# Kernel optimization log

Measured on AMD Instinct MI355X. Metric: run time of the kernel, lower is better.

Reference implementation:

```python
import jax, jax.numpy as jnp
import numpy as np

B, T, D, H, NHASH, BS, L, DFF = 4, 4096, 512, 8, 4, 64, 4, 2048
DH = D // H           # 64
NB = T // BS          # 64 buckets per hash round
MASK_VAL = -5e4       # TOKEN_SELF_ATTN_VALUE from reformer-pytorch


def setup_inputs() -> dict:
    key = jax.random.key(0)
    ks = jax.random.split(key, 8)
    s = D ** -0.5
    return {
        "src": jax.random.normal(ks[0], (B, T, D), jnp.float32),
        "rotations": jax.random.normal(ks[1], (L, DH, NHASH, NB // 2), jnp.float32),
        "Wqk": jax.random.normal(ks[2], (L, D, D), jnp.float32) * s,
        "Wv": jax.random.normal(ks[3], (L, D, D), jnp.float32) * s,
        "Wout": jax.random.normal(ks[4], (L, D, D), jnp.float32) * s,
        "bout": jnp.zeros((L, D), jnp.float32),
        "W1": jax.random.normal(ks[5], (L, DFF, D), jnp.float32) * s,
        "b1": jnp.zeros((L, DFF), jnp.float32),
        "W2": jax.random.normal(ks[6], (L, D, DFF), jnp.float32) * (DFF ** -0.5),
        "b2": jnp.zeros((L, D), jnp.float32),
        "g2": jnp.ones((L, D), jnp.float32),
        "be2": jnp.zeros((L, D), jnp.float32),
        "gf": jnp.ones((D,), jnp.float32),
        "bf": jnp.zeros((D,), jnp.float32),
    }


def _ln(x, g, b, eps=1e-6):
    m = x.mean(-1, keepdims=True)
    v = ((x - m) ** 2).mean(-1, keepdims=True)
    return (x - m) * jax.lax.rsqrt(v + eps) * g + b


def _look_one_back(x):
    # concat each chunk with the previous chunk along the within-chunk axis
    return jnp.concatenate([x, jnp.roll(x, 1, axis=1)], axis=2)


def _lsh_attention(qk, v, rot):
    # qk, v: (bh, T, DH); rot: (DH, NHASH, NB//2). Shared-QK LSH attention.
    bh = qk.shape[0]
    rotated = jnp.einsum('btf,fhr->bhtr', qk, rot)               # (bh,NHASH,T,NB/2)
    full = jnp.concatenate([rotated, -rotated], axis=-1)          # (bh,NHASH,T,NB)
    buckets = jnp.argmax(full, axis=-1)                           # (bh,NHASH,T)
    buckets = buckets + (jnp.arange(NHASH) * NB)[None, :, None]   # offset per round
    buckets = buckets.reshape(bh, NHASH * T)

    ticker = jnp.arange(NHASH * T)
    bt = buckets * T + (ticker % T)                               # unique sort keys
    sticker = jnp.argsort(bt, axis=-1)                            # sort positions
    undo = jnp.argsort(sticker, axis=-1)
    st = sticker % T                                              # original positions

    sqk = jnp.take_along_axis(qk, st[..., None], axis=1)          # (bh,NHASH*T,DH)
    sv = jnp.take_along_axis(v, st[..., None], axis=1)

    C = NHASH * NB                                                # chunks
    bq_t = st.reshape(bh, C, BS)
    bqk = sqk.reshape(bh, C, BS, DH)
    bv = sv.reshape(bh, C, BS, DH)

    bq = bqk
    bk = bqk / jnp.maximum(jnp.linalg.norm(bqk, axis=-1, keepdims=True), 1e-12)
    bk = _look_one_back(bk)                                       # (bh,C,2*BS,DH)
    bv = _look_one_back(bv)
    bkv_t = _look_one_back(bq_t)                                  # (bh,C,2*BS)

    dots = jnp.einsum('bcie,bcje->bcij', bq, bk) * (DH ** -0.5)   # (bh,C,BS,2BS)
    self_mask = bq_t[:, :, :, None] == bkv_t[:, :, None, :]
    dots = jnp.where(self_mask, MASK_VAL, dots)

    lse = jax.scipy.special.logsumexp(dots, axis=-1, keepdims=True)
    probs = jnp.exp(dots - lse)
    bo = jnp.einsum('bcij,bcje->bcie', probs, bv)                 # (bh,C,BS,DH)

    so = bo.reshape(bh, NHASH * T, DH)
    slog = lse.reshape(bh, NHASH * T)
    o = jnp.take_along_axis(so, undo[..., None], axis=1).reshape(bh, NHASH, T, DH)
    lg = jnp.take_along_axis(slog, undo, axis=1).reshape(bh, NHASH, T, 1)
    w = jnp.exp(lg - jax.scipy.special.logsumexp(lg, axis=1, keepdims=True))
    return jnp.sum(o * w, axis=1)                                 # (bh,T,DH)


def _split_heads(x):
    return x.reshape(B, T, H, DH).transpose(0, 2, 1, 3).reshape(B * H, T, DH)


def _merge_heads(x):
    return x.reshape(B, H, T, DH).transpose(0, 2, 1, 3).reshape(B, T, D)


def reference(src, rotations, Wqk, Wv, Wout, bout, W1, b1, W2, b2, g2, be2, gf, bf):
    x = src
    for i in range(L):
        # LSH self-attention (post-norm path: norm1 is never applied in source)
        qk = _split_heads(x @ Wqk[i].T)
        v = _split_heads(x @ Wv[i].T)
        att = _merge_heads(_lsh_attention(qk, v, rotations[i]))
        att = att @ Wout[i].T + bout[i]
        x = x + att
        # positionalwise FFN + residual + norm2
        ff = jax.nn.relu(x @ W1[i].T + b1[i]) @ W2[i].T + b2[i]
        x = _ln(x + ff, g2[i], be2[i])
    return _ln(x, gf, bf)
```

## Files before the change

kernel.cpp:

```cpp
#include <hip/hip_runtime.h>
#include <math.h>

#define TT    4096
#define DD    512
#define HH    8
#define DHH   64
#define NH    4
#define LLAY  4
#define DFFN  2048
#define BHH   32
#define NC    256
#define MROWS 16384

typedef __attribute__((ext_vector_type(8))) short s16x8;
typedef __attribute__((ext_vector_type(4))) float f32x4;
typedef unsigned short ushort_t;

union U4 { unsigned u[4]; s16x8 v; };

__device__ __forceinline__ unsigned short f2bf(float f) {
    unsigned u = __float_as_uint(f);
    unsigned r = (u + 0x7FFFu + ((u >> 16) & 1u)) >> 16;
    return (unsigned short)r;
}
__device__ __forceinline__ float bf2f(unsigned short h) {
    return __uint_as_float(((unsigned)h) << 16);
}

__device__ __forceinline__ void xcd_swz(int& bx, int& by) {
    const int gx = gridDim.x;
    const int nwg = gx * gridDim.y;
    const int flat = by * gx + bx;
    const int q = nwg >> 3;
    const int swz = (flat & 7) * q + (flat >> 3);
    bx = swz % gx;
    by = swz / gx;
}

__global__ __launch_bounds__(256) void gemm_bf3_k(
    const ushort_t* __restrict__ Ah, const ushort_t* __restrict__ Al, int lda,
    const ushort_t* __restrict__ Wh, const ushort_t* __restrict__ Wl,
    const float* __restrict__ bias, const float* __restrict__ resid,
    float* __restrict__ outf, ushort_t* __restrict__ outh, ushort_t* __restrict__ outl,
    int M, int N, int K, int relu)
{
    __shared__ __align__(16) ushort_t lds[4 * 128 * 32];
    const int tid  = threadIdx.x;
    const int lane = tid & 63;
    const int wv   = tid >> 6;
    const int wm   = wv >> 1, wn = wv & 1;
    int bx = blockIdx.x, by = blockIdx.y;
    xcd_swz(bx, by);
    const int row0 = by * 128, col0 = bx * 128;
    const int g    = lane >> 4;

    f32x4 acc[4][4];
#pragma unroll
    for (int mi = 0; mi < 4; mi++)
#pragma unroll
        for (int ni = 0; ni < 4; ni++) acc[mi][ni] = (f32x4)(0.f);

    const int srow0 = wv * 32;

    for (int k0 = 0; k0 < K; k0 += 32) {
        __syncthreads();
#pragma unroll
        for (int ii = 0; ii < 2; ii++) {
            const int r   = srow0 + ii * 16 + (lane >> 2);
            const int ug  = (((lane & 3) ^ ((r >> 1) & 3)) << 3);
            const size_t ga = (size_t)(row0 + r) * lda + k0 + ug;
            const size_t gw = (size_t)(col0 + r) * K   + k0 + ug;
            const int lo  = (srow0 + ii * 16) * 32;
            __builtin_amdgcn_global_load_lds(
                (const __attribute__((address_space(1))) void*)(Ah + ga),
                (__attribute__((address_space(3))) void*)&lds[0 * 4096 + lo], 16, 0, 0);
            __builtin_amdgcn_global_load_lds(
                (const __attribute__((address_space(1))) void*)(Al + ga),
                (__attribute__((address_space(3))) void*)&lds[1 * 4096 + lo], 16, 0, 0);
            __builtin_amdgcn_global_load_lds(
                (const __attribute__((address_space(1))) void*)(Wh + gw),
                (__attribute__((address_space(3))) void*)&lds[2 * 4096 + lo], 16, 0, 0);
            __builtin_amdgcn_global_load_lds(
                (const __attribute__((address_space(1))) void*)(Wl + gw),
                (__attribute__((address_space(3))) void*)&lds[3 * 4096 + lo], 16, 0, 0);
        }
        __syncthreads();

        s16x8 ah[4], al[4], wh[4], wl[4];
#pragma unroll
        for (int mi = 0; mi < 4; mi++) {
            const int m  = wm * 64 + mi * 16 + (lane & 15);
            const int pu = ((g ^ ((m >> 1) & 3)) << 3);
            ah[mi] = *(const s16x8*)&lds[0 * 4096 + m * 32 + pu];
            al[mi] = *(const s16x8*)&lds[1 * 4096 + m * 32 + pu];
            const int n  = wn * 64 + mi * 16 + (lane & 15);
            const int pn = ((g ^ ((n >> 1) & 3)) << 3);
            wh[mi] = *(const s16x8*)&lds[2 * 4096 + n * 32 + pn];
            wl[mi] = *(const s16x8*)&lds[3 * 4096 + n * 32 + pn];
        }
#pragma unroll
        for (int mi = 0; mi < 4; mi++)
#pragma unroll
            for (int ni = 0; ni < 4; ni++) {
                acc[mi][ni] = __builtin_amdgcn_mfma_f32_16x16x32_bf16(ah[mi], wh[ni], acc[mi][ni], 0, 0, 0);
                acc[mi][ni] = __builtin_amdgcn_mfma_f32_16x16x32_bf16(al[mi], wh[ni], acc[mi][ni], 0, 0, 0);
                acc[mi][ni] = __builtin_amdgcn_mfma_f32_16x16x32_bf16(ah[mi], wl[ni], acc[mi][ni], 0, 0, 0);
            }
    }

#pragma unroll
    for (int mi = 0; mi < 4; mi++) {
#pragma unroll
        for (int ni = 0; ni < 4; ni++) {
#pragma unroll
            for (int r = 0; r < 4; r++) {
                const int row = row0 + wm * 64 + mi * 16 + g * 4 + r;
                const int col = col0 + wn * 64 + ni * 16 + (lane & 15);
                float v = acc[mi][ni][r];
                if (bias)  v += bias[col];
                if (relu)  v = fmaxf(v, 0.f);
                if (resid) v += resid[(size_t)row * N + col];
                if (outf)  outf[(size_t)row * N + col] = v;
                if (outh) {
                    unsigned short h = f2bf(v);
                    outh[(size_t)row * N + col] = h;
                    outl[(size_t)row * N + col] = f2bf(v - bf2f(h));
                }
            }
        }
    }
}

__global__ __launch_bounds__(256) void gemm_bf6_k(
    const ushort_t* __restrict__ A1, const ushort_t* __restrict__ A2,
    const ushort_t* __restrict__ A3, int lda,
    const ushort_t* __restrict__ W1, const ushort_t* __restrict__ W2,
    const ushort_t* __restrict__ W3,
    float* __restrict__ outf, int M, int N, int K)
{
    __shared__ __align__(16) ushort_t lds[6 * 128 * 32];
    const int tid  = threadIdx.x;
    const int lane = tid & 63;
    const int wv   = tid >> 6;
    const int wm   = wv >> 1, wn = wv & 1;
    int bx = blockIdx.x, by = blockIdx.y;
    xcd_swz(bx, by);
    const int row0 = by * 128, col0 = bx * 128;
    const int g    = lane >> 4;

    f32x4 acc[4][4];
#pragma unroll
    for (int mi = 0; mi < 4; mi++)
#pragma unroll
        for (int ni = 0; ni < 4; ni++) acc[mi][ni] = (f32x4)(0.f);

    const int srow0 = wv * 32;

    for (int k0 = 0; k0 < K; k0 += 32) {
        __syncthreads();
#pragma unroll
        for (int ii = 0; ii < 2; ii++) {
            const int r   = srow0 + ii * 16 + (lane >> 2);
            const int ug  = (((lane & 3) ^ ((r >> 1) & 3)) << 3);
            const size_t ga = (size_t)(row0 + r) * lda + k0 + ug;
            const size_t gw = (size_t)(col0 + r) * K   + k0 + ug;
            const int lo  = (srow0 + ii * 16) * 32;
            __builtin_amdgcn_global_load_lds(
                (const __attribute__((address_space(1))) void*)(A1 + ga),
                (__attribute__((address_space(3))) void*)&lds[0 * 4096 + lo], 16, 0, 0);
            __builtin_amdgcn_global_load_lds(
                (const __attribute__((address_space(1))) void*)(A2 + ga),
                (__attribute__((address_space(3))) void*)&lds[1 * 4096 + lo], 16, 0, 0);
            __builtin_amdgcn_global_load_lds(
                (const __attribute__((address_space(1))) void*)(A3 + ga),
                (__attribute__((address_space(3))) void*)&lds[2 * 4096 + lo], 16, 0, 0);
            __builtin_amdgcn_global_load_lds(
                (const __attribute__((address_space(1))) void*)(W1 + gw),
                (__attribute__((address_space(3))) void*)&lds[3 * 4096 + lo], 16, 0, 0);
            __builtin_amdgcn_global_load_lds(
                (const __attribute__((address_space(1))) void*)(W2 + gw),
                (__attribute__((address_space(3))) void*)&lds[4 * 4096 + lo], 16, 0, 0);
            __builtin_amdgcn_global_load_lds(
                (const __attribute__((address_space(1))) void*)(W3 + gw),
                (__attribute__((address_space(3))) void*)&lds[5 * 4096 + lo], 16, 0, 0);
        }
        __syncthreads();

        s16x8 a1[4], a2[4], a3[4], w1[4], w2[4], w3[4];
#pragma unroll
        for (int mi = 0; mi < 4; mi++) {
            const int m  = wm * 64 + mi * 16 + (lane & 15);
            const int pu = ((g ^ ((m >> 1) & 3)) << 3);
            a1[mi] = *(const s16x8*)&lds[0 * 4096 + m * 32 + pu];
            a2[mi] = *(const s16x8*)&lds[1 * 4096 + m * 32 + pu];
            a3[mi] = *(const s16x8*)&lds[2 * 4096 + m * 32 + pu];
            const int n  = wn * 64 + mi * 16 + (lane & 15);
            const int pn = ((g ^ ((n >> 1) & 3)) << 3);
            w1[mi] = *(const s16x8*)&lds[3 * 4096 + n * 32 + pn];
            w2[mi] = *(const s16x8*)&lds[4 * 4096 + n * 32 + pn];
            w3[mi] = *(const s16x8*)&lds[5 * 4096 + n * 32 + pn];
        }
#pragma unroll
        for (int mi = 0; mi < 4; mi++)
#pragma unroll
            for (int ni = 0; ni < 4; ni++) {
                acc[mi][ni] = __builtin_amdgcn_mfma_f32_16x16x32_bf16(a1[mi], w1[ni], acc[mi][ni], 0, 0, 0);
                acc[mi][ni] = __builtin_amdgcn_mfma_f32_16x16x32_bf16(a2[mi], w1[ni], acc[mi][ni], 0, 0, 0);
                acc[mi][ni] = __builtin_amdgcn_mfma_f32_16x16x32_bf16(a1[mi], w2[ni], acc[mi][ni], 0, 0, 0);
                acc[mi][ni] = __builtin_amdgcn_mfma_f32_16x16x32_bf16(a2[mi], w2[ni], acc[mi][ni], 0, 0, 0);
                acc[mi][ni] = __builtin_amdgcn_mfma_f32_16x16x32_bf16(a1[mi], w3[ni], acc[mi][ni], 0, 0, 0);
                acc[mi][ni] = __builtin_amdgcn_mfma_f32_16x16x32_bf16(a3[mi], w1[ni], acc[mi][ni], 0, 0, 0);
            }
    }

#pragma unroll
    for (int mi = 0; mi < 4; mi++) {
#pragma unroll
        for (int ni = 0; ni < 4; ni++) {
#pragma unroll
            for (int r = 0; r < 4; r++) {
                const int row = row0 + wm * 64 + mi * 16 + g * 4 + r;
                const int col = col0 + wn * 64 + ni * 16 + (lane & 15);
                outf[(size_t)row * N + col] = acc[mi][ni][r];
            }
        }
    }
}

__global__ __launch_bounds__(256) void cvt_k(
    const float* __restrict__ in, ushort_t* __restrict__ o1,
    ushort_t* __restrict__ o2, ushort_t* __restrict__ o3, int n4)
{
    int i = blockIdx.x * 256 + threadIdx.x;
    if (i >= n4) return;
    float4 v = ((const float4*)in)[i];
    float vv[4] = {v.x, v.y, v.z, v.w};
    union { unsigned short us[4]; ushort4 v4; } H, L, M;
#pragma unroll
    for (int q = 0; q < 4; q++) {
        unsigned short a = f2bf(vv[q]);
        float r1 = vv[q] - bf2f(a);
        unsigned short b = f2bf(r1);
        H.us[q] = a; L.us[q] = b;
        M.us[q] = f2bf(r1 - bf2f(b));
    }
    ((ushort4*)o1)[i] = H.v4;
    ((ushort4*)o2)[i] = L.v4;
    if (o3) ((ushort4*)o3)[i] = M.v4;
}

__global__ __launch_bounds__(256) void bucket_k(
    const float* __restrict__ qk, const float* __restrict__ rot,
    int* __restrict__ bkt)
{
    __shared__ float rs[NH][64][32];
    const int bh = blockIdx.y;
    const int t = blockIdx.x * 256 + threadIdx.x;
    for (int i = threadIdx.x; i < NH * 64 * 32; i += 256) {
        int r = i >> 11, f = (i >> 5) & 63, j = i & 31;
        rs[r][f][j] = rot[(f * NH + r) * 32 + j];
    }
    __syncthreads();
    const int b = bh >> 3, h = bh & 7;
    const float* q = qk + ((size_t)(b * TT + t)) * DD + h * DHH;
    float qv[64];
#pragma unroll
    for (int f4 = 0; f4 < 16; f4++) {
        float4 tmp = ((const float4*)q)[f4];
        qv[f4 * 4 + 0] = tmp.x; qv[f4 * 4 + 1] = tmp.y;
        qv[f4 * 4 + 2] = tmp.z; qv[f4 * 4 + 3] = tmp.w;
    }
    for (int r = 0; r < NH; r++) {
        float rv[32];
#pragma unroll
        for (int j = 0; j < 32; j++) rv[j] = 0.f;
        for (int f = 0; f < 64; f++) {
            float qf = qv[f];
#pragma unroll
            for (int j = 0; j < 32; j++) rv[j] = fmaf(qf, rs[r][f][j], rv[j]);
        }
        float best = rv[0];
        int bi = 0;
#pragma unroll
        for (int j = 1; j < 32; j++) { if (rv[j] > best) { best = rv[j]; bi = j; } }
#pragma unroll
        for (int j = 0; j < 32; j++) { float v = -rv[j]; if (v > best) { best = v; bi = 32 + j; } }
        bkt[((size_t)bh * NH + r) * TT + t] = bi;
    }
}

__global__ __launch_bounds__(256) void sort_k(
    const int* __restrict__ bkt, int* __restrict__ st)
{
    __shared__ int lb[TT];
    __shared__ unsigned short cnt[128][64];
    __shared__ int base[64];
    const int r = blockIdx.x, bh = blockIdx.y;
    const int tid = threadIdx.x;
    const int* src = bkt + ((size_t)bh * NH + r) * TT;

    const int4* s4 = (const int4*)src;
    int4* l4 = (int4*)lb;
#pragma unroll
    for (int q = 0; q < 4; q++) l4[tid + q * 256] = s4[tid + q * 256];
    unsigned* cz = (unsigned*)cnt;
#pragma unroll
    for (int q = 0; q < 16; q++) cz[tid + q * 256] = 0;
    __syncthreads();

    if (tid < 128) {
        for (int it = 0; it < 32; it++) {
            int bb = lb[tid * 32 + it];
            cnt[tid][bb]++;
        }
    }
    __syncthreads();

    if (tid < 64) {
        const int bb = tid;
        int run = 0;
        for (int s = 0; s < 128; s++) {
            int t = cnt[s][bb];
            cnt[s][bb] = (unsigned short)run;
            run += t;
        }
        int inc = run;
#pragma unroll
        for (int off = 1; off < 64; off <<= 1) {
            int n = __shfl_up(inc, off, 64);
            if (tid >= off) inc += n;
        }
        base[bb] = inc - run;
    }
    __syncthreads();

    if (tid < 128) {
        int* dst = st + (size_t)bh * (NH * TT) + (size_t)r * TT;
        for (int it = 0; it < 32; it++) {
            int t = tid * 32 + it;
            int bb = lb[t];
            int pos = base[bb] + (int)cnt[tid][bb];
            cnt[tid][bb]++;
            dst[pos] = t;
        }
    }
}

__global__ __launch_bounds__(256, 2) void attn_k(
    const float* __restrict__ qk, const float* __restrict__ vbuf,
    const int* __restrict__ st, float* __restrict__ obuf,
    float* __restrict__ lseb, int bh0)
{
    __shared__ __align__(16) ushort_t ksh[128 * 72];
    __shared__ __align__(16) ushort_t ksl[128 * 72];
    __shared__ __align__(16) unsigned vsp[128 * 66];
    __shared__ float invn[128];
    __shared__ int   tks[128];

    const int c   = blockIdx.x;
    const int bhl = blockIdx.y;
    const int bh  = bh0 + bhl;
    const int b   = bh >> 3, h = bh & 7;
    const int tid = threadIdx.x;
    const int* stb = st + (size_t)bh * (NH * TT);

    if (tid < 128) {
        int cc = (tid < 64) ? c : ((c + NC - 1) & (NC - 1));
        tks[tid] = stb[cc * 64 + (tid & 63)];
    }
    __syncthreads();

    {
        const int row = tid >> 1, c0 = (tid & 1) * 32;
        const int t = tks[row];
        const float4* kg = (const float4*)(qk + ((size_t)(b * TT + t)) * DD + h * DHH + c0);
        const float4* vg = (const float4*)(vbuf + ((size_t)(b * TT + t)) * DD + h * DHH + c0);
        float kv[32], vv[32];
        float ss = 0.f;
#pragma unroll
        for (int q = 0; q < 8; q++) {
            float4 kq = kg[q], vq = vg[q];
            kv[4 * q + 0] = kq.x; kv[4 * q + 1] = kq.y; kv[4 * q + 2] = kq.z; kv[4 * q + 3] = kq.w;
            vv[4 * q + 0] = vq.x; vv[4 * q + 1] = vq.y; vv[4 * q + 2] = vq.z; vv[4 * q + 3] = vq.w;
            ss += kq.x * kq.x + kq.y * kq.y + kq.z * kq.z + kq.w * kq.w;
        }
        ss += __shfl_xor(ss, 1);
        if ((tid & 1) == 0) invn[row] = 1.0f / fmaxf(sqrtf(ss), 1e-12f);

        unsigned hw[16], lw[16];
#pragma unroll
        for (int e = 0; e < 16; e++) {
            float a = kv[2 * e], b2 = kv[2 * e + 1];
            unsigned short ha = f2bf(a), hb = f2bf(b2);
            hw[e] = (unsigned)ha | ((unsigned)hb << 16);
            lw[e] = (unsigned)f2bf(a - bf2f(ha)) | ((unsigned)f2bf(b2 - bf2f(hb)) << 16);
        }
        uint4* kdh = (uint4*)&ksh[row * 72 + c0];
        uint4* kdl = (uint4*)&ksl[row * 72 + c0];
#pragma unroll
        for (int q = 0; q < 4; q++) {
            kdh[q] = make_uint4(hw[4 * q], hw[4 * q + 1], hw[4 * q + 2], hw[4 * q + 3]);
            kdl[q] = make_uint4(lw[4 * q], lw[4 * q + 1], lw[4 * q + 2], lw[4 * q + 3]);
        }
        unsigned pw[32];
#pragma unroll
        for (int e = 0; e < 32; e++) {
            unsigned short hv = f2bf(vv[e]);
            pw[e] = (unsigned)hv | ((unsigned)f2bf(vv[e] - bf2f(hv)) << 16);
        }
        uint2* vd = (uint2*)&vsp[row * 66 + c0];
#pragma unroll
        for (int q = 0; q < 16; q++) vd[q] = make_uint2(pw[2 * q], pw[2 * q + 1]);
    }
    __syncthreads();

    const int lane = tid & 63;
    const int wv   = tid >> 6;
    const int cc16 = lane & 15;
    const int g    = lane >> 4;
    const int rr   = c >> 6;

    f32x4 stt[8];
#pragma unroll
    for (int jt = 0; jt < 8; jt++) stt[jt] = (f32x4)(0.f);

    const int qrow = wv * 16 + cc16;
#pragma unroll
    for (int ks = 0; ks < 2; ks++) {
        s16x8 qh = *(const s16x8*)&ksh[qrow * 72 + ks * 32 + g * 8];
        s16x8 ql = *(const s16x8*)&ksl[qrow * 72 + ks * 32 + g * 8];
#pragma unroll
        for (int jt = 0; jt < 8; jt++) {
            const int krow = jt * 16 + cc16;
            s16x8 ah = *(const s16x8*)&ksh[krow * 72 + ks * 32 + g * 8];
            s16x8 al = *(const s16x8*)&ksl[krow * 72 + ks * 32 + g * 8];
            stt[jt] = __builtin_amdgcn_mfma_f32_16x16x32_bf16(ah, qh, stt[jt], 0, 0, 0);
            stt[jt] = __builtin_amdgcn_mfma_f32_16x16x32_bf16(al, qh, stt[jt], 0, 0, 0);
            stt[jt] = __builtin_amdgcn_mfma_f32_16x16x32_bf16(ah, ql, stt[jt], 0, 0, 0);
        }
    }

    const int tqi = tks[wv * 16 + cc16];
    float m = -INFINITY;
#pragma unroll
    for (int jt = 0; jt < 8; jt++) {
#pragma unroll
        for (int r4 = 0; r4 < 4; r4++) {
            const int j = jt * 16 + g * 4 + r4;
            float d = stt[jt][r4] * invn[j] * 0.125f;
            if (tqi == tks[j]) d = -5e4f;
            stt[jt][r4] = d;
            m = fmaxf(m, d);
        }
    }
    m = fmaxf(m, __shfl_xor(m, 16));
    m = fmaxf(m, __shfl_xor(m, 32));
    float s = 0.f;
#pragma unroll
    for (int jt = 0; jt < 8; jt++) {
#pragma unroll
        for (int r4 = 0; r4 < 4; r4++) {
            float e = expf(stt[jt][r4] - m);
            stt[jt][r4] = e;
            s += e;
        }
    }
    s += __shfl_xor(s, 16);
    s += __shfl_xor(s, 32);
    const float is = 1.0f / s;
    if (g == 0) lseb[((size_t)bh * NH + rr) * TT + tqi] = m + logf(s);

    unsigned ph[8][2], pl[8][2];
#pragma unroll
    for (int jt = 0; jt < 8; jt++) {
#pragma unroll
        for (int w2 = 0; w2 < 2; w2++) {
            float p0 = stt[jt][2 * w2] * is;
            float p1 = stt[jt][2 * w2 + 1] * is;
            unsigned short h0 = f2bf(p0), h1 = f2bf(p1);
            ph[jt][w2] = (unsigned)h0 | ((unsigned)h1 << 16);
            pl[jt][w2] = (unsigned)f2bf(p0 - bf2f(h0)) | ((unsigned)f2bf(p1 - bf2f(h1)) << 16);
        }
    }

    f32x4 occ[4];
#pragma unroll
    for (int nt = 0; nt < 4; nt++) occ[nt] = (f32x4)(0.f);

    const int srcLow  = ((g & 1) << 5) + cc16;
    const int srcHigh = srcLow + 16;
    const bool hiT = (lane & 32) != 0;

#pragma unroll
    for (int ks = 0; ks < 4; ks++) {
        U4 Phi, Plo;
        {
            unsigned a0 = (unsigned)__shfl((int)ph[2 * ks][0], srcLow);
            unsigned a1 = (unsigned)__shfl((int)ph[2 * ks][1], srcLow);
            unsigned a2 = (unsigned)__shfl((int)ph[2 * ks][0], srcHigh);
            unsigned a3 = (unsigned)__shfl((int)ph[2 * ks][1], srcHigh);
            unsigned b0 = (unsigned)__shfl((int)ph[2 * ks + 1][0], srcLow);
            unsigned b1 = (unsigned)__shfl((int)ph[2 * ks + 1][1], srcLow);
            unsigned b2 = (unsigned)__shfl((int)ph[2 * ks + 1][0], srcHigh);
            unsigned b3 = (unsigned)__shfl((int)ph[2 * ks + 1][1], srcHigh);
            Phi.u[0] = hiT ? b0 : a0; Phi.u[1] = hiT ? b1 : a1;
            Phi.u[2] = hiT ? b2 : a2; Phi.u[3] = hiT ? b3 : a3;
            unsigned c0 = (unsigned)__shfl((int)pl[2 * ks][0], srcLow);
            unsigned c1 = (unsigned)__shfl((int)pl[2 * ks][1], srcLow);
            unsigned c2 = (unsigned)__shfl((int)pl[2 * ks][0], srcHigh);
            unsigned c3 = (unsigned)__shfl((int)pl[2 * ks][1], srcHigh);
            unsigned d0 = (unsigned)__shfl((int)pl[2 * ks + 1][0], srcLow);
            unsigned d1 = (unsigned)__shfl((int)pl[2 * ks + 1][1], srcLow);
            unsigned d2 = (unsigned)__shfl((int)pl[2 * ks + 1][0], srcHigh);
            unsigned d3 = (unsigned)__shfl((int)pl[2 * ks + 1][1], srcHigh);
            Plo.u[0] = hiT ? d0 : c0; Plo.u[1] = hiT ? d1 : c1;
            Plo.u[2] = hiT ? d2 : c2; Plo.u[3] = hiT ? d3 : c3;
        }
#pragma unroll
        for (int nt = 0; nt < 4; nt++) {
            unsigned u[8];
#pragma unroll
            for (int e = 0; e < 8; e++)
                u[e] = vsp[(32 * ks + 8 * g + e) * 66 + nt * 16 + cc16];
            U4 Vh, Vl;
#pragma unroll
            for (int m2 = 0; m2 < 4; m2++) {
                Vh.u[m2] = (u[2 * m2] & 0xffffu) | (u[2 * m2 + 1] << 16);
                Vl.u[m2] = (u[2 * m2] >> 16) | (u[2 * m2 + 1] & 0xffff0000u);
            }
            occ[nt] = __builtin_amdgcn_mfma_f32_16x16x32_bf16(Phi.v, Vh.v, occ[nt], 0, 0, 0);
            occ[nt] = __builtin_amdgcn_mfma_f32_16x16x32_bf16(Plo.v, Vh.v, occ[nt], 0, 0, 0);
            occ[nt] = __builtin_amdgcn_mfma_f32_16x16x32_bf16(Phi.v, Vl.v, occ[nt], 0, 0, 0);
        }
    }

#pragma unroll
    for (int r4 = 0; r4 < 4; r4++) {
        const int i = wv * 16 + g * 4 + r4;
        const int ti = tks[i];
        float* dst = obuf + (((size_t)bhl * NH + rr) * TT + ti) * DHH + cc16;
        dst[0]  = occ[0][r4];
        dst[16] = occ[1][r4];
        dst[32] = occ[2][r4];
        dst[48] = occ[3][r4];
    }
}

__global__ __launch_bounds__(256) void combine_k(
    const float* __restrict__ obuf, const float* __restrict__ lseb,
    ushort_t* __restrict__ att, int bh0)
{
    int idx = blockIdx.x * 256 + threadIdx.x;
    int d = idx & 63;
    int t = (idx >> 6) & (TT - 1);
    int bhl = idx >> 18;
    int bh = bh0 + bhl;
    float l0 = lseb[((size_t)bh * NH + 0) * TT + t];
    float l1 = lseb[((size_t)bh * NH + 1) * TT + t];
    float l2 = lseb[((size_t)bh * NH + 2) * TT + t];
    float l3 = lseb[((size_t)bh * NH + 3) * TT + t];
    float m = fmaxf(fmaxf(l0, l1), fmaxf(l2, l3));
    float e0 = expf(l0 - m), e1 = expf(l1 - m), e2 = expf(l2 - m), e3 = expf(l3 - m);
    float inv = 1.0f / (e0 + e1 + e2 + e3);
    float o0 = obuf[(((size_t)bhl * NH + 0) * TT + t) * DHH + d];
    float o1 = obuf[(((size_t)bhl * NH + 1) * TT + t) * DHH + d];
    float o2 = obuf[(((size_t)bhl * NH + 2) * TT + t) * DHH + d];
    float o3 = obuf[(((size_t)bhl * NH + 3) * TT + t) * DHH + d];
    float o = (e0 * o0 + e1 * o1 + e2 * o2 + e3 * o3) * inv;
    int b = bh >> 3, h = bh & 7;
    size_t base = (size_t)(b * TT + t) * 1024 + h * DHH + d;
    unsigned short hi = f2bf(o);
    att[base]       = hi;
    att[base + 512] = f2bf(o - bf2f(hi));
}

__global__ __launch_bounds__(64) void ln_k(
    const float* __restrict__ in, const float* __restrict__ g,
    const float* __restrict__ be, float* __restrict__ out,
    ushort_t* __restrict__ oh, ushort_t* __restrict__ ol,
    ushort_t* __restrict__ ol2)
{
    const int row = blockIdx.x;
    const int tid = threadIdx.x;
    const float* x = in + (size_t)row * DD;
    float4 a = *(const float4*)(x + tid * 8);
    float4 b = *(const float4*)(x + tid * 8 + 4);
    float s = a.x + a.y + a.z + a.w + b.x + b.y + b.z + b.w;
#pragma unroll
    for (int o = 32; o >= 1; o >>= 1) s += __shfl_xor(s, o, 64);
    float mean = s * (1.0f / 512.0f);
    float dx[8];
    dx[0] = a.x - mean; dx[1] = a.y - mean; dx[2] = a.z - mean; dx[3] = a.w - mean;
    dx[4] = b.x - mean; dx[5] = b.y - mean; dx[6] = b.z - mean; dx[7] = b.w - mean;
    float ss = 0.f;
#pragma unroll
    for (int q = 0; q < 8; q++) ss += dx[q] * dx[q];
#pragma unroll
    for (int o = 32; o >= 1; o >>= 1) ss += __shfl_xor(ss, o, 64);
    float var = ss * (1.0f / 512.0f);
    float inv = 1.0f / sqrtf(var + 1e-6f);
    const float* gp = g + tid * 8;
    const float* bp = be + tid * 8;
    float y[8];
#pragma unroll
    for (int q = 0; q < 8; q++) y[q] = dx[q] * inv * gp[q] + bp[q];
    float* yp = out + (size_t)row * DD + tid * 8;
    *(float4*)(yp)     = make_float4(y[0], y[1], y[2], y[3]);
    *(float4*)(yp + 4) = make_float4(y[4], y[5], y[6], y[7]);
    if (oh) {
        union { unsigned short us[8]; ushort4 v4[2]; } H, L, M;
#pragma unroll
        for (int q = 0; q < 8; q++) {
            unsigned short h = f2bf(y[q]);
            float r1 = y[q] - bf2f(h);
            unsigned short l = f2bf(r1);
            H.us[q] = h; L.us[q] = l;
            M.us[q] = f2bf(r1 - bf2f(l));
        }
        size_t e = (size_t)row * DD + tid * 8;
        *(ushort4*)(oh + e)      = H.v4[0];
        *(ushort4*)(oh + e + 4)  = H.v4[1];
        *(ushort4*)(ol + e)      = L.v4[0];
        *(ushort4*)(ol + e + 4)  = L.v4[1];
        *(ushort4*)(ol2 + e)     = M.v4[0];
        *(ushort4*)(ol2 + e + 4) = M.v4[1];
    }
}

extern "C" void kernel_launch(void* const* d_in, const int* in_sizes, int n_in,
                              void* d_out, int out_size, void* d_ws, size_t ws_size,
                              hipStream_t stream)
{
    const float* src  = (const float*)d_in[0];
    const float* rots = (const float*)d_in[1];
    const float* Wqk  = (const float*)d_in[2];
    const float* Wv   = (const float*)d_in[3];
    const float* Wout = (const float*)d_in[4];
    const float* bout = (const float*)d_in[5];
    const float* W1   = (const float*)d_in[6];
    const float* b1   = (const float*)d_in[7];
    const float* W2   = (const float*)d_in[8];
    const float* b2   = (const float*)d_in[9];
    const float* g2   = (const float*)d_in[10];
    const float* be2  = (const float*)d_in[11];
    const float* gf   = (const float*)d_in[12];
    const float* bf   = (const float*)d_in[13];
    float* out = (float*)d_out;

    char* w = (char*)d_ws;
    const size_t SZ_X = (size_t)MROWS * DD * 4;
    const size_t XHALF = (size_t)MROWS * DD;
    float*    x     = (float*)(w);
    ushort_t* xs    = (ushort_t*)(w + SZ_X);
    ushort_t* xh    = xs;
    ushort_t* xl    = xs + XHALF;
    ushort_t* xl2   = xs + 2 * XHALF;
    char*     p     = w + SZ_X + 3 * XHALF * 2;
    float*    qkb   = (float*)(p);
    ushort_t* attb  = (ushort_t*)(p);
    float*    vb    = (float*)(p + SZ_X);
    float*    obuf  = (float*)(p + 2 * SZ_X);
    ushort_t* h1b   = (ushort_t*)(p + 2 * SZ_X);
    ushort_t* wb    = (ushort_t*)(p + 4 * SZ_X);
    char*     tail  = p + 4 * SZ_X + 6029312 * 2;
    int*      bkt   = (int*)(tail);
    int*      st    = (int*)(tail + (size_t)BHH * NH * TT * 4);
    float*    lseb  = (float*)(tail + 2 * (size_t)BHH * NH * TT * 4);

    ushort_t* wvh = wb;            ushort_t* wvl = wb + 262144;
    ushort_t* woh = wb + 524288;   ushort_t* wol = wb + 786432;
    ushort_t* w1h = wb + 1048576;  ushort_t* w1l = wb + 2097152;
    ushort_t* w2h = wb + 3145728;  ushort_t* w2l = wb + 4194304;
    ushort_t* wq1 = wb + 5242880;  ushort_t* wq2 = wb + 5505024;
    ushort_t* wq3 = wb + 5767168;
    const size_t H1HALF = (size_t)8192 * DFFN;
    ushort_t* h1h = h1b;           ushort_t* h1l = h1b + H1HALF;

    hipMemcpyAsync(x, src, SZ_X, hipMemcpyDeviceToDevice, stream);
    cvt_k<<<(MROWS * DD / 4 + 255) / 256, 256, 0, stream>>>(src, xh, xl, xl2, MROWS * DD / 4);

    for (int i = 0; i < LLAY; i++) {
        const float* Wqk_i = Wqk + (size_t)i * DD * DD;
        const float* Wv_i  = Wv  + (size_t)i * DD * DD;
        const float* Wout_i= Wout+ (size_t)i * DD * DD;
        const float* bout_i= bout+ (size_t)i * DD;
        const float* W1_i  = W1  + (size_t)i * DFFN * DD;
        const float* b1_i  = b1  + (size_t)i * DFFN;
        const float* W2_i  = W2  + (size_t)i * DD * DFFN;
        const float* b2_i  = b2  + (size_t)i * DD;
        const float* g2_i  = g2  + (size_t)i * DD;
        const float* be2_i = be2 + (size_t)i * DD;
        const float* rot_i = rots + (size_t)i * DHH * NH * 32;

        cvt_k<<<(262144 / 4 + 255) / 256, 256, 0, stream>>>(Wqk_i, wq1, wq2, wq3, 262144 / 4);
        cvt_k<<<(262144 / 4 + 255) / 256, 256, 0, stream>>>(Wv_i, wvh, wvl, nullptr, 262144 / 4);
        cvt_k<<<(262144 / 4 + 255) / 256, 256, 0, stream>>>(Wout_i, woh, wol, nullptr, 262144 / 4);
        cvt_k<<<(1048576 / 4 + 255) / 256, 256, 0, stream>>>(W1_i, w1h, w1l, nullptr, 1048576 / 4);
        cvt_k<<<(1048576 / 4 + 255) / 256, 256, 0, stream>>>(W2_i, w2h, w2l, nullptr, 1048576 / 4);

        gemm_bf6_k<<<dim3(4, 128), 256, 0, stream>>>(xh, xl, xl2, DD, wq1, wq2, wq3,
                                                     qkb, MROWS, DD, DD);
        gemm_bf3_k<<<dim3(4, 128), 256, 0, stream>>>(xh, xl, DD, wvh, wvl,
                                                     nullptr, nullptr, vb, nullptr, nullptr,
                                                     MROWS, DD, DD, 0);
        bucket_k<<<dim3(16, BHH), 256, 0, stream>>>(qkb, rot_i, bkt);
        sort_k<<<dim3(NH, BHH), 256, 0, stream>>>(bkt, st);

        for (int s = 0; s < 2; s++) {
            attn_k<<<dim3(NC, 16), 256, 0, stream>>>(qkb, vb, st, obuf, lseb, s * 16);
            combine_k<<<16384, 256, 0, stream>>>(obuf, lseb, attb, s * 16);
        }

        gemm_bf3_k<<<dim3(4, 128), 256, 0, stream>>>(attb, attb + 512, 1024, woh, wol,
                                                     bout_i, x, x, xh, xl,
                                                     MROWS, DD, DD, 0);
        for (int s = 0; s < 2; s++) {
            const size_t ro = (size_t)s * 8192;
            gemm_bf3_k<<<dim3(16, 64), 256, 0, stream>>>(xh + ro * DD, xl + ro * DD, DD,
                                                         w1h, w1l, b1_i, nullptr,
                                                         nullptr, h1h, h1l,
                                                         8192, DFFN, DD, 1);
            gemm_bf3_k<<<dim3(4, 64), 256, 0, stream>>>(h1h, h1l, DFFN, w2h, w2l,
                                                        b2_i, x + ro * DD,
                                                        vb + ro * DD, nullptr, nullptr,
                                                        8192, DD, DFFN, 0);
        }
        ln_k<<<MROWS, 64, 0, stream>>>(vb, g2_i, be2_i, x, xh, xl, xl2);
    }
    ln_k<<<MROWS, 64, 0, stream>>>(x, gf, bf, out, nullptr, nullptr, nullptr);
}
```

Before: 3.461 ms.

## Split FFN along hidden dimension instead of rows, accumulating second GEMM via residual

The FFN was previously processed in two row halves (8192 rows each, full DFF). It now splits the hidden dimension into two 1024-wide halves over all 16384 rows. The second GEMM of the second half adds onto the first half's output through the residual input. A new leading-dimension parameter for the weight matrix allows strided access into W2 columns. This gives the second GEMM larger grids (4x128 instead of 4x64), which aims to improve occupancy for the K-heavy W2 GEMM. The cost is an extra read-modify-write pass of the fp32 output and a different summation order.

```diff
diff --git a/kernel.cpp b/kernel.cpp
--- a/kernel.cpp
+++ b/kernel.cpp
@@ -39,7 +39,7 @@
 
 __global__ __launch_bounds__(256) void gemm_bf3_k(
     const ushort_t* __restrict__ Ah, const ushort_t* __restrict__ Al, int lda,
-    const ushort_t* __restrict__ Wh, const ushort_t* __restrict__ Wl,
+    const ushort_t* __restrict__ Wh, const ushort_t* __restrict__ Wl, int ldw,
     const float* __restrict__ bias, const float* __restrict__ resid,
     float* __restrict__ outf, ushort_t* __restrict__ outh, ushort_t* __restrict__ outl,
     int M, int N, int K, int relu)
@@ -69,7 +69,7 @@
             const int r   = srow0 + ii * 16 + (lane >> 2);
             const int ug  = (((lane & 3) ^ ((r >> 1) & 3)) << 3);
             const size_t ga = (size_t)(row0 + r) * lda + k0 + ug;
-            const size_t gw = (size_t)(col0 + r) * K   + k0 + ug;
+            const size_t gw = (size_t)(col0 + r) * ldw + k0 + ug;
             const int lo  = (srow0 + ii * 16) * 32;
             __builtin_amdgcn_global_load_lds(
                 (const __attribute__((address_space(1))) void*)(Ah + ga),
@@ -673,7 +673,7 @@
     ushort_t* w2h = wb + 3145728;  ushort_t* w2l = wb + 4194304;
     ushort_t* wq1 = wb + 5242880;  ushort_t* wq2 = wb + 5505024;
     ushort_t* wq3 = wb + 5767168;
-    const size_t H1HALF = (size_t)8192 * DFFN;
+    const size_t H1HALF = (size_t)MROWS * 1024;
     ushort_t* h1h = h1b;           ushort_t* h1l = h1b + H1HALF;
 
     hipMemcpyAsync(x, src, SZ_X, hipMemcpyDeviceToDevice, stream);
@@ -700,7 +700,7 @@
 
         gemm_bf6_k<<<dim3(4, 128), 256, 0, stream>>>(xh, xl, xl2, DD, wq1, wq2, wq3,
                                                      qkb, MROWS, DD, DD);
-        gemm_bf3_k<<<dim3(4, 128), 256, 0, stream>>>(xh, xl, DD, wvh, wvl,
+        gemm_bf3_k<<<dim3(4, 128), 256, 0, stream>>>(xh, xl, DD, wvh, wvl, DD,
                                                      nullptr, nullptr, vb, nullptr, nullptr,
                                                      MROWS, DD, DD, 0);
         bucket_k<<<dim3(16, BHH), 256, 0, stream>>>(qkb, rot_i, bkt);
@@ -711,19 +711,22 @@
             combine_k<<<16384, 256, 0, stream>>>(obuf, lseb, attb, s * 16);
         }
 
-        gemm_bf3_k<<<dim3(4, 128), 256, 0, stream>>>(attb, attb + 512, 1024, woh, wol,
+        gemm_bf3_k<<<dim3(4, 128), 256, 0, stream>>>(attb, attb + 512, 1024, woh, wol, DD,
                                                      bout_i, x, x, xh, xl,
                                                      MROWS, DD, DD, 0);
-        for (int s = 0; s < 2; s++) {
-            const size_t ro = (size_t)s * 8192;
-            gemm_bf3_k<<<dim3(16, 64), 256, 0, stream>>>(xh + ro * DD, xl + ro * DD, DD,
-                                                         w1h, w1l, b1_i, nullptr,
+        for (int hf = 0; hf < 2; hf++) {
+            const size_t wo = (size_t)hf * 1024;
+            gemm_bf3_k<<<dim3(8, 128), 256, 0, stream>>>(xh, xl, DD,
+                                                         w1h + wo * DD, w1l + wo * DD, DD,
+                                                         b1_i + wo, nullptr,
                                                          nullptr, h1h, h1l,
-                                                         8192, DFFN, DD, 1);
-            gemm_bf3_k<<<dim3(4, 64), 256, 0, stream>>>(h1h, h1l, DFFN, w2h, w2l,
-                                                        b2_i, x + ro * DD,
-                                                        vb + ro * DD, nullptr, nullptr,
-                                                        8192, DD, DFFN, 0);
+                                                         MROWS, 1024, DD, 1);
+            gemm_bf3_k<<<dim3(4, 128), 256, 0, stream>>>(h1h, h1l, 1024,
+                                                         w2h + wo, w2l + wo, DFFN,
+                                                         hf == 0 ? b2_i : nullptr,
+                                                         hf == 0 ? x : vb,
+                                                         vb, nullptr, nullptr,
+                                                         MROWS, DD, 1024, 0);
         }
         ln_k<<<MROWS, 64, 0, stream>>>(vb, g2_i, be2_i, x, xh, xl, xl2);
     }
```

Measured after the change: 3.212 ms. 7.2% less time.
